# Optimization experiments

Hardware: AMD Instinct MI355X
Metric: run time of the kernel (lower is better)

Reference implementation:

```python
import jax, jax.numpy as jnp
import numpy as np

B, S, HID = 4, 2048, 768
H, DBLK, HD = 12, 256, 64  # heads, block_dim = HID//3, head_dim


def setup_inputs() -> dict:
    key = jax.random.key(0)
    ks = jax.random.split(key, 7)
    scale = 0.02
    return {
        "inputs": jax.random.normal(ks[0], (B, S, HID), jnp.float32),
        "Wq": jax.random.normal(ks[1], (H, DBLK, HD), jnp.float32) * scale,
        "bq": jax.random.normal(ks[2], (H, HD), jnp.float32) * scale,
        "Wk": jax.random.normal(ks[3], (H, DBLK, HD), jnp.float32) * scale,
        "bk": jax.random.normal(ks[4], (H, HD), jnp.float32) * scale,
        "Wv": jax.random.normal(ks[5], (H, DBLK, HD), jnp.float32) * scale,
        "bv": jax.random.normal(ks[6], (H, HD), jnp.float32) * scale,
    }


def reference(inputs, Wq, bq, Wk, bk, Wv, bv):
    b, s, hid = inputs.shape
    h, dblk, hd = Wq.shape
    hpm = h // 3  # heads per modality
    # split hidden into 3 modality blocks: [B, S, 3, DBLK]
    xm = inputs.reshape(b, s, 3, dblk)

    def proj(W, bias):
        # block-diagonal GEMM: each modality's x projected by its hpm heads
        y = jnp.einsum('bsmd,mhde->bmhse', xm, W.reshape(3, hpm, dblk, hd))
        y = y + bias.reshape(3, hpm, 1, hd)
        return y.reshape(b, h, s, hd)

    Q = proj(Wq, bq)
    K = proj(Wk, bk)
    V = proj(Wv, bv)

    scores = jnp.einsum('bhse,bhte->bhst', Q, K) / jnp.sqrt(jnp.float32(hd))
    probs = jax.nn.softmax(scores, axis=-1)  # dropout p=0 -> identity
    ctx = jnp.einsum('bhst,bhte->bhse', probs, V)
    # concat heads along feature dim: [B, S, H*HD]
    return ctx.transpose(0, 2, 1, 3).reshape(b, s, h * hd)
```

## Files before the change

### kernel.cpp

```cpp
#include <hip/hip_runtime.h>
#include <hip/hip_bf16.h>

#define B_    4
#define S_    2048
#define HID_  768
#define H_    12
#define DBLK_ 256
#define HD_   64
#define BH_   (B_ * H_)
#define QSZ_  (B_ * H_ * S_ * HD_)
#define WTSZ_ (3 * H_ * HD_ * DBLK_)

typedef _Float16 f16x4 __attribute__((ext_vector_type(4)));
typedef _Float16 f16x8 __attribute__((ext_vector_type(8)));
typedef float    f32x4 __attribute__((ext_vector_type(4)));
typedef float    f32x16 __attribute__((ext_vector_type(16)));

#if __has_builtin(__builtin_amdgcn_exp2f)
#define EXP2(x) __builtin_amdgcn_exp2f(x)
#else
#define EXP2(x) exp2f(x)
#endif

typedef const void __attribute__((address_space(1)))* gptr_t;
typedef       void __attribute__((address_space(3)))* sptr_t;

__global__ __launch_bounds__(256) void wconv(
    const float* __restrict__ Wq, const float* __restrict__ Wk,
    const float* __restrict__ Wv, _Float16* __restrict__ whf)
{
    const int idx  = blockIdx.x * 256 + threadIdx.x;
    const int j    = idx & 7;
    const int lane = (idx >> 3) & 63;
    const int et   = (idx >> 9) & 1;
    const int kk   = (idx >> 10) & 7;
    const int eh   = (idx >> 13) & 1;
    const int ph   = idx >> 14;
    const int h    = ph % H_;
    const int p    = ph / H_;
    const int e = eh * 32 + et * 16 + (lane & 15);
    const int k = kk * 32 + (lane >> 4) * 8 + j;
    const float* W = (p == 0) ? Wq : (p == 1) ? Wk : Wv;
    whf[idx] = (_Float16)W[((size_t)h * DBLK_ + k) * HD_ + e];
}

__global__ __launch_bounds__(256, 3) void qkv_proj(
    const float* __restrict__ x, const _Float16* __restrict__ whf,
    const float* __restrict__ bq, const float* __restrict__ bk,
    const float* __restrict__ bv,
    _Float16* __restrict__ qo, _Float16* __restrict__ khf,
    _Float16* __restrict__ vtf)
{
    const int i   = blockIdx.x;
    const int g   = i >> 7;
    const int sc  = i & 127;
    const int m   = g >> 1;
    const int s0g = sc * 64;

    const int tid  = threadIdx.x;
    const int lane = tid & 63;
    const int w    = tid >> 6;
    const int ln   = lane & 15;
    const int qd   = lane >> 4;
    const int h    = 2 * g + (w >> 1);
    const int eh   = w & 1;

    __shared__ _Float16 xs[64 * 256];

    {
        const int rr   = tid >> 6;
        const int c4   = tid & 63;
        const int g16  = c4 >> 1;
        const int half = c4 & 1;
        #pragma unroll
        for (int pass = 0; pass < 16; pass++) {
            const int r = pass * 4 + rr;
            const float4 v = *(const float4*)(
                x + (size_t)(s0g + r) * HID_ + m * DBLK_ + c4 * 4);
            f16x4 hv;
            hv[0] = (_Float16)v.x; hv[1] = (_Float16)v.y;
            hv[2] = (_Float16)v.z; hv[3] = (_Float16)v.w;
            *(f16x4*)(xs + r * 256 + ((g16 ^ (r & 7)) * 8) + half * 4) = hv;
        }
    }
    __syncthreads();

    f32x4 acc[3][2][4];
    #pragma unroll
    for (int p = 0; p < 3; p++)
        #pragma unroll
        for (int et = 0; et < 2; et++)
            #pragma unroll
            for (int st = 0; st < 4; st++)
                acc[p][et][st] = (f32x4){0.f, 0.f, 0.f, 0.f};

    const _Float16* wb = whf + (size_t)((h * 2 + eh) * 16) * 512 + lane * 8;

    for (int kk = 0; kk < 8; kk++) {
        f16x8 a[4];
        #pragma unroll
        for (int st = 0; st < 4; st++)
            a[st] = *(const f16x8*)(
                xs + (st * 16 + ln) * 256 + (((kk * 4 + qd) ^ (ln & 7)) * 8));
        #pragma unroll
        for (int p = 0; p < 3; p++)
            #pragma unroll
            for (int et = 0; et < 2; et++) {
                const f16x8 bb = *(const f16x8*)(
                    wb + (size_t)p * 196608 + (kk * 2 + et) * 512);
                #pragma unroll
                for (int st = 0; st < 4; st++)
                    acc[p][et][st] = __builtin_amdgcn_mfma_f32_16x16x32_f16(
                        a[st], bb, acc[p][et][st], 0, 0, 0);
            }
    }

    const float QS = 0.18033688011112042f;
    const int b    = s0g >> 11;
    const int s0   = s0g & 2047;
    const int bhh  = b * H_ + h;
    const int tile = s0 >> 6;
    const int ht   = w >> 1;

    __syncthreads();
    {
        _Float16* qtile = xs + ht * 4096;
        _Float16* ktile = xs + 8192 + ht * 4096;
        const size_t tbv = (size_t)(bhh * 32 + tile) * 4096;
        #pragma unroll
        for (int et = 0; et < 2; et++) {
            const int d  = eh * 32 + et * 16 + ln;
            const int dc = d >> 3, d7 = d & 7;
            const float biasq = bq[h * HD_ + d];
            const float biask = bk[h * HD_ + d];
            const float biasv = bv[h * HD_ + d];
            #pragma unroll
            for (int st = 0; st < 4; st++) {
                f16x4 vv;
                #pragma unroll
                for (int r = 0; r < 4; r++) vv[r] = (_Float16)(acc[2][et][st][r] + biasv);
                const int vc = st * 2 + (qd >> 1);
                *(f16x4*)(vtf + tbv + d * 64 + ((vc ^ d7) * 8) + (qd & 1) * 4) = vv;
                #pragma unroll
                for (int r = 0; r < 4; r++) {
                    const int sl  = st * 16 + qd * 4 + r;
                    const int rho = st * 16 + (qd & 1) * 8 + (qd >> 1) * 4 + r;
                    qtile[sl  * 64 + ((dc ^ (sl  & 7)) * 8) + d7] =
                        (_Float16)((acc[0][et][st][r] + biasq) * QS);
                    ktile[rho * 64 + ((dc ^ (rho & 7)) * 8) + d7] =
                        (_Float16)(acc[1][et][st][r] + biask);
                }
            }
        }
    }
    __syncthreads();
    #pragma unroll
    for (int it = 0; it < 4; it++) {
        const int idx  = it * 256 + tid;
        const int ht2  = idx >> 9;
        const int rest = idx & 511;
        const int row  = rest >> 3;
        const int c    = rest & 7;
        const int bhh2 = b * H_ + 2 * g + ht2;
        const f16x8 qv = *(const f16x8*)(xs + ht2 * 4096 + row * 64 + ((c ^ (row & 7)) * 8));
        *(f16x8*)(qo + ((size_t)bhh2 * S_ + s0 + row) * HD_ + c * 8) = qv;
        const f16x8 kv8 = *(const f16x8*)(xs + 8192 + ht2 * 4096 + row * 64 + c * 8);
        *(f16x8*)(khf + (size_t)(bhh2 * 32 + tile) * 4096 + row * 64 + c * 8) = kv8;
    }
}

__global__ __launch_bounds__(256, 3) void attn(
    const _Float16* __restrict__ qh, const _Float16* __restrict__ khf,
    const _Float16* __restrict__ vtf, float* __restrict__ out)
{
    const int i    = blockIdx.x;
    const int slot = i >> 3;
    const int bh   = (i & 7) * 6 + (slot % 6);
    const int qt   = slot / 6;
    const int h = bh % H_, b = bh / H_;
    const int q0 = qt * 128;

    const int tid  = threadIdx.x;
    const int lane = tid & 63;
    const int w    = tid >> 6;
    const int l5   = lane & 31;
    const int g    = lane >> 5;
    const int x7   = l5 & 7;

    __shared__ __align__(16) char lds[2][16384];

    f16x8 qf[4];
    {
        const _Float16* qb = qh + ((size_t)bh * S_ + q0 + w * 32 + l5) * HD_;
        #pragma unroll
        for (int kk = 0; kk < 4; kk++)
            qf[kk] = *(const f16x8*)(qb + kk * 16 + g * 8);
    }

    f32x16 o[2];
    #pragma unroll
    for (int dt = 0; dt < 2; dt++)
        #pragma unroll
        for (int r = 0; r < 16; r++) o[dt][r] = 0.f;
    float lp[4] = {0.f, 0.f, 0.f, 0.f};

    const char* kbase = (const char*)(khf + (size_t)bh * 32 * 4096);
    const char* vbase = (const char*)(vtf + (size_t)bh * 32 * 4096);
    const int   seg   = w * 1024 + lane * 16;
    const int   wseg  = w * 1024;

    auto dma = [&](int it, int buf) {
        const char* ks = kbase + (size_t)it * 8192;
        const char* vs = vbase + (size_t)it * 8192;
        char* lk = &lds[buf][0];
        char* lv = &lds[buf][8192];
        #pragma unroll
        for (int q = 0; q < 2; q++) {
            __builtin_amdgcn_global_load_lds(
                (gptr_t)(ks + q * 4096 + seg), (sptr_t)(lk + q * 4096 + wseg), 16, 0, 0);
            __builtin_amdgcn_global_load_lds(
                (gptr_t)(vs + q * 4096 + seg), (sptr_t)(lv + q * 4096 + wseg), 16, 0, 0);
        }
    };

    dma(0, 0);

    for (int it = 0; it < 32; it++) {
        const int buf = it & 1;
        __syncthreads();
        if (it + 1 < 32) dma(it + 1, buf ^ 1);

        const char* lk = &lds[buf][0];
        const char* lv = &lds[buf][8192];

        f16x8 kf[2][4];
        #pragma unroll
        for (int mt = 0; mt < 2; mt++)
            #pragma unroll
            for (int kk = 0; kk < 4; kk++)
                kf[mt][kk] = *(const f16x8*)(
                    lk + (mt * 32 + l5) * 128 + (((kk * 2 + g) ^ x7) * 16));
        f16x8 vf[2][4];
        #pragma unroll
        for (int dt = 0; dt < 2; dt++)
            #pragma unroll
            for (int ks = 0; ks < 4; ks++)
                vf[dt][ks] = *(const f16x8*)(
                    lv + (dt * 32 + l5) * 128 + (((ks * 2 + g) ^ x7) * 16));

        f32x16 c[2];
        #pragma unroll
        for (int mt = 0; mt < 2; mt++) {
            #pragma unroll
            for (int r = 0; r < 16; r++) c[mt][r] = 0.f;
            #pragma unroll
            for (int kk = 0; kk < 4; kk++)
                c[mt] = __builtin_amdgcn_mfma_f32_32x32x16_f16(
                    kf[mt][kk], qf[kk], c[mt], 0, 0, 0);
        }

        f16x8 a[4];
        #pragma unroll
        for (int ks = 0; ks < 4; ks++) {
            float e[8];
            #pragma unroll
            for (int j = 0; j < 8; j++) {
                e[j] = EXP2(c[ks >> 1][(ks & 1) * 8 + j]);
                a[ks][j] = (_Float16)e[j];
            }
            lp[ks] += ((e[0] + e[1]) + (e[2] + e[3]))
                    + ((e[4] + e[5]) + (e[6] + e[7]));
        }

        #pragma unroll
        for (int dt = 0; dt < 2; dt++)
            #pragma unroll
            for (int ks = 0; ks < 4; ks++)
                o[dt] = __builtin_amdgcn_mfma_f32_32x32x16_f16(
                    a[ks], vf[dt][ks], o[dt], 0, 0, 0);
    }

    float lf = (lp[0] + lp[1]) + (lp[2] + lp[3]);
    lf += __shfl_xor(lf, 32, 64);
    float* lsc = (float*)(void*)&lds[0][0] + w * 64;
    lsc[lane] = 1.f / lf;
    __syncthreads();
    #pragma unroll
    for (int r = 0; r < 16; r++) {
        const int qrow = (r & 3) + 8 * (r >> 2) + 4 * g;
        const float li = lsc[qrow];
        float* op = out + ((size_t)b * S_ + q0 + w * 32 + qrow) * HID_
                  + (size_t)h * HD_ + l5;
        op[0]  = o[0][r] * li;
        op[32] = o[1][r] * li;
    }
}

extern "C" void kernel_launch(void* const* d_in, const int* in_sizes, int n_in,
                              void* d_out, int out_size, void* d_ws, size_t ws_size,
                              hipStream_t stream) {
    const float* x  = (const float*)d_in[0];
    const float* Wq = (const float*)d_in[1];
    const float* bq = (const float*)d_in[2];
    const float* Wk = (const float*)d_in[3];
    const float* bk = (const float*)d_in[4];
    const float* Wv = (const float*)d_in[5];
    const float* bv = (const float*)d_in[6];
    float* out = (float*)d_out;

    _Float16* q  = (_Float16*)d_ws;
    _Float16* k  = q + QSZ_;
    _Float16* vt = k + QSZ_;
    const size_t need = ((size_t)3 * QSZ_ + WTSZ_) * sizeof(_Float16);
    _Float16* wh = (ws_size >= need) ? (vt + QSZ_)
                                     : (_Float16*)d_out;

    wconv<<<WTSZ_ / 256, 256, 0, stream>>>(Wq, Wk, Wv, wh);
    qkv_proj<<<768, 256, 0, stream>>>(x, wh, bq, bk, bv, q, k, vt);
    attn<<<768, 256, 0, stream>>>(q, k, vt, out);
}
```

Measured before the change: 160.2 us.

## Split KV tile across warp pairs, each warp handling two query subtiles

Changes the attention work split. Each of the four warps used to own 32 query rows against the whole 64-key tile. Now warps are arranged 2x2: each covers 64 query rows (two 32-row subtiles) against half of the key tile. This halves the K and V fragments each warp reads from LDS per iteration and reuses each K fragment across two query subtiles. The cost is more accumulator registers (four f32x16 output blocks) and an epilogue that merges the two partial softmax sums and partial outputs through LDS with extra barriers.

```diff
diff --git a/kernel.cpp b/kernel.cpp
--- a/kernel.cpp
+++ b/kernel.cpp
@@ -183,26 +183,32 @@
     const int tid  = threadIdx.x;
     const int lane = tid & 63;
     const int w    = tid >> 6;
+    const int wk   = w >> 1;
+    const int wq   = w & 1;
     const int l5   = lane & 31;
     const int g    = lane >> 5;
     const int x7   = l5 & 7;
 
     __shared__ __align__(16) char lds[2][16384];
 
-    f16x8 qf[4];
-    {
-        const _Float16* qb = qh + ((size_t)bh * S_ + q0 + w * 32 + l5) * HD_;
+    f16x8 qf[2][4];
+    #pragma unroll
+    for (int qt2 = 0; qt2 < 2; qt2++) {
+        const _Float16* qb = qh +
+            ((size_t)bh * S_ + q0 + wq * 64 + qt2 * 32 + l5) * HD_;
         #pragma unroll
         for (int kk = 0; kk < 4; kk++)
-            qf[kk] = *(const f16x8*)(qb + kk * 16 + g * 8);
-    }
-
-    f32x16 o[2];
-    #pragma unroll
-    for (int dt = 0; dt < 2; dt++)
-        #pragma unroll
-        for (int r = 0; r < 16; r++) o[dt][r] = 0.f;
-    float lp[4] = {0.f, 0.f, 0.f, 0.f};
+            qf[qt2][kk] = *(const f16x8*)(qb + kk * 16 + g * 8);
+    }
+
+    f32x16 o[2][2];
+    #pragma unroll
+    for (int qt2 = 0; qt2 < 2; qt2++)
+        #pragma unroll
+        for (int dt = 0; dt < 2; dt++)
+            #pragma unroll
+            for (int r = 0; r < 16; r++) o[qt2][dt][r] = 0.f;
+    float lp[2] = {0.f, 0.f};
 
     const char* kbase = (const char*)(khf + (size_t)bh * 32 * 4096);
     const char* vbase = (const char*)(vtf + (size_t)bh * 32 * 4096);
@@ -233,66 +239,109 @@
         const char* lk = &lds[buf][0];
         const char* lv = &lds[buf][8192];
 
-        f16x8 kf[2][4];
-        #pragma unroll
-        for (int mt = 0; mt < 2; mt++)
+        f16x8 kf[4];
+        #pragma unroll
+        for (int kk = 0; kk < 4; kk++)
+            kf[kk] = *(const f16x8*)(
+                lk + (wk * 32 + l5) * 128 + (((kk * 2 + g) ^ x7) * 16));
+        f16x8 vf[2][2];
+        #pragma unroll
+        for (int dt = 0; dt < 2; dt++)
+            #pragma unroll
+            for (int ks = 0; ks < 2; ks++)
+                vf[dt][ks] = *(const f16x8*)(
+                    lv + (dt * 32 + l5) * 128 + (((wk * 4 + ks * 2 + g) ^ x7) * 16));
+
+        #pragma unroll
+        for (int qt2 = 0; qt2 < 2; qt2++) {
+            f32x16 c;
+            #pragma unroll
+            for (int r = 0; r < 16; r++) c[r] = 0.f;
             #pragma unroll
             for (int kk = 0; kk < 4; kk++)
-                kf[mt][kk] = *(const f16x8*)(
-                    lk + (mt * 32 + l5) * 128 + (((kk * 2 + g) ^ x7) * 16));
-        f16x8 vf[2][4];
-        #pragma unroll
-        for (int dt = 0; dt < 2; dt++)
-            #pragma unroll
-            for (int ks = 0; ks < 4; ks++)
-                vf[dt][ks] = *(const f16x8*)(
-                    lv + (dt * 32 + l5) * 128 + (((ks * 2 + g) ^ x7) * 16));
-
-        f32x16 c[2];
-        #pragma unroll
-        for (int mt = 0; mt < 2; mt++) {
-            #pragma unroll
-            for (int r = 0; r < 16; r++) c[mt][r] = 0.f;
-            #pragma unroll
-            for (int kk = 0; kk < 4; kk++)
-                c[mt] = __builtin_amdgcn_mfma_f32_32x32x16_f16(
-                    kf[mt][kk], qf[kk], c[mt], 0, 0, 0);
-        }
-
-        f16x8 a[4];
-        #pragma unroll
-        for (int ks = 0; ks < 4; ks++) {
-            float e[8];
-            #pragma unroll
-            for (int j = 0; j < 8; j++) {
-                e[j] = EXP2(c[ks >> 1][(ks & 1) * 8 + j]);
-                a[ks][j] = (_Float16)e[j];
+                c = __builtin_amdgcn_mfma_f32_32x32x16_f16(
+                    kf[kk], qf[qt2][kk], c, 0, 0, 0);
+
+            f16x8 a[2];
+            #pragma unroll
+            for (int ks = 0; ks < 2; ks++) {
+                float e[8];
+                #pragma unroll
+                for (int j = 0; j < 8; j++) {
+                    e[j] = EXP2(c[ks * 8 + j]);
+                    a[ks][j] = (_Float16)e[j];
+                }
+                lp[qt2] += ((e[0] + e[1]) + (e[2] + e[3]))
+                         + ((e[4] + e[5]) + (e[6] + e[7]));
             }
-            lp[ks] += ((e[0] + e[1]) + (e[2] + e[3]))
-                    + ((e[4] + e[5]) + (e[6] + e[7]));
-        }
-
-        #pragma unroll
-        for (int dt = 0; dt < 2; dt++)
-            #pragma unroll
-            for (int ks = 0; ks < 4; ks++)
-                o[dt] = __builtin_amdgcn_mfma_f32_32x32x16_f16(
-                    a[ks], vf[dt][ks], o[dt], 0, 0, 0);
-    }
-
-    float lf = (lp[0] + lp[1]) + (lp[2] + lp[3]);
-    lf += __shfl_xor(lf, 32, 64);
-    float* lsc = (float*)(void*)&lds[0][0] + w * 64;
-    lsc[lane] = 1.f / lf;
-    __syncthreads();
-    #pragma unroll
-    for (int r = 0; r < 16; r++) {
-        const int qrow = (r & 3) + 8 * (r >> 2) + 4 * g;
-        const float li = lsc[qrow];
-        float* op = out + ((size_t)b * S_ + q0 + w * 32 + qrow) * HID_
-                  + (size_t)h * HD_ + l5;
-        op[0]  = o[0][r] * li;
-        op[32] = o[1][r] * li;
+
+            #pragma unroll
+            for (int dt = 0; dt < 2; dt++)
+                #pragma unroll
+                for (int ks = 0; ks < 2; ks++)
+                    o[qt2][dt] = __builtin_amdgcn_mfma_f32_32x32x16_f16(
+                        a[ks], vf[dt][ks], o[qt2][dt], 0, 0, 0);
+        }
+    }
+
+    float lf[2];
+    #pragma unroll
+    for (int qt2 = 0; qt2 < 2; qt2++)
+        lf[qt2] = lp[qt2] + __shfl_xor(lp[qt2], 32, 64);
+
+    __syncthreads();
+    float* lbuf = (float*)(void*)&lds[0][0];
+    if (wk == 1 && lane < 32) {
+        lbuf[(wq * 2 + 0) * 32 + l5] = lf[0];
+        lbuf[(wq * 2 + 1) * 32 + l5] = lf[1];
+    }
+    __syncthreads();
+    if (wk == 0 && lane < 32) {
+        const float t0 = lf[0] + lbuf[(wq * 2 + 0) * 32 + l5];
+        const float t1 = lf[1] + lbuf[(wq * 2 + 1) * 32 + l5];
+        lbuf[(wq * 2 + 0) * 32 + l5] = 1.f / t0;
+        lbuf[(wq * 2 + 1) * 32 + l5] = 1.f / t1;
+    }
+
+    char* obuf = &lds[0][1024];
+    #pragma unroll
+    for (int qt2 = 0; qt2 < 2; qt2++) {
+        __syncthreads();
+        if (wk == 1) {
+            #pragma unroll
+            for (int dt = 0; dt < 2; dt++)
+                #pragma unroll
+                for (int p = 0; p < 4; p++) {
+                    f32x4 v4;
+                    v4[0] = o[qt2][dt][4 * p + 0];
+                    v4[1] = o[qt2][dt][4 * p + 1];
+                    v4[2] = o[qt2][dt][4 * p + 2];
+                    v4[3] = o[qt2][dt][4 * p + 3];
+                    *(f32x4*)(obuf + (wq * 2 + dt) * 4096 + p * 1024 + lane * 16) = v4;
+                }
+        }
+        __syncthreads();
+        if (wk == 0) {
+            #pragma unroll
+            for (int dt = 0; dt < 2; dt++) {
+                #pragma unroll
+                for (int p = 0; p < 4; p++) {
+                    const f32x4 v4 = *(const f32x4*)(
+                        obuf + (wq * 2 + dt) * 4096 + p * 1024 + lane * 16);
+                    o[qt2][dt][4 * p + 0] += v4[0];
+                    o[qt2][dt][4 * p + 1] += v4[1];
+                    o[qt2][dt][4 * p + 2] += v4[2];
+                    o[qt2][dt][4 * p + 3] += v4[3];
+                }
+                #pragma unroll
+                for (int r = 0; r < 16; r++) {
+                    const int qrow = (r & 3) + 8 * (r >> 2) + 4 * g;
+                    const float li = lbuf[(wq * 2 + qt2) * 32 + qrow];
+                    out[((size_t)b * S_ + q0 + wq * 64 + qt2 * 32 + qrow) * HID_
+                        + (size_t)h * HD_ + dt * 32 + l5] = o[qt2][dt][r] * li;
+                }
+            }
+        }
     }
 }
 
```

Measured after the change: 167.8 us. 4.8% more time.
